# Kernel optimization log

Hardware: AMD Instinct MI355X
Metric: run time of the kernel (lower is better)

The kernel has to match this reference:

```python
import jax, jax.numpy as jnp
import numpy as np

T, B, IN, H, OUT, L = 2048, 128, 64, 128, 32, 2


def setup_inputs() -> dict:
    key = jax.random.key(0)
    ks = jax.random.split(key, 8)
    s_in = 1.0 / np.sqrt(H)  # torch LSTM init scale: U(-1/sqrt(H), 1/sqrt(H))
    inp = {
        "x": jax.random.normal(ks[0], (T, B, IN), dtype=jnp.float32),
        "w_ih0": jax.random.uniform(ks[1], (4 * H, IN), minval=-s_in, maxval=s_in, dtype=jnp.float32),
        "w_hh0": jax.random.uniform(ks[2], (4 * H, H), minval=-s_in, maxval=s_in, dtype=jnp.float32),
        "w_ih1": jax.random.uniform(ks[3], (4 * H, H), minval=-s_in, maxval=s_in, dtype=jnp.float32),
        "w_hh1": jax.random.uniform(ks[4], (4 * H, H), minval=-s_in, maxval=s_in, dtype=jnp.float32),
        "fc_w": jax.random.uniform(ks[5], (OUT, H), minval=-s_in, maxval=s_in, dtype=jnp.float32),
        "fc_b": jax.random.uniform(ks[6], (OUT,), minval=-s_in, maxval=s_in, dtype=jnp.float32),
    }
    return inp


def _lstm_layer(x, w_ih, w_hh):
    # x: [T, B, D]; gate order i, f, g, o (PyTorch convention), no bias.
    x_proj = jnp.einsum("tbd,gd->tbg", x, w_ih)  # [T, B, 4H] precomputed input GEMM
    h0 = jnp.zeros((x.shape[1], H), dtype=x.dtype)
    c0 = jnp.zeros((x.shape[1], H), dtype=x.dtype)

    def step(carry, xp):
        h, c = carry
        gates = xp + h @ w_hh.T  # [B, 4H]
        i, f, g, o = jnp.split(gates, 4, axis=-1)
        i = jax.nn.sigmoid(i)
        f = jax.nn.sigmoid(f)
        g = jnp.tanh(g)
        o = jax.nn.sigmoid(o)
        c = f * c + i * g
        h = o * jnp.tanh(c)
        return (h, c), h

    (h_n, c_n), ys = jax.lax.scan(step, (h0, c0), x_proj)
    return ys, h_n, c_n


def reference(x, w_ih0, w_hh0, w_ih1, w_hh1, fc_w, fc_b):
    y0, h0n, c0n = _lstm_layer(x, w_ih0, w_hh0)
    y1, h1n, c1n = _lstm_layer(y0, w_ih1, w_hh1)
    out = jnp.einsum("tbh,oh->tbo", y1, fc_w) + fc_b  # [T, B, OUT]
    h_n = jnp.stack([h0n, h1n], axis=0)  # [L, B, H]
    c_n = jnp.stack([c0n, c1n], axis=0)
    return out, (h_n, c_n)
```

## Files before the change

### kernel.cpp

```cpp
#include <hip/hip_runtime.h>

#define T_ 2048
#define B_ 128
#define IN_ 64
#define H_ 128
#define OUT_ 32
#define CH_ 32
#define RING_ 2

typedef _Float16 half8 __attribute__((ext_vector_type(8)));
typedef _Float16 half4v __attribute__((ext_vector_type(4)));
typedef float float4v __attribute__((ext_vector_type(4)));

#define XSTR 144
#define HSTR 272
#define GRP_ELEMS ((size_t)RING_ * CH_ * 16 * 128)
#define RING_BYTES ((size_t)8 * GRP_ELEMS * 2)

#define NLOG2E  (-1.4426950408889634f)
#define C2LOG2E ( 2.8853900817779268f)

__device__ __forceinline__ float exp2_hw(float x) {
#if __has_builtin(__builtin_amdgcn_exp2f)
  return __builtin_amdgcn_exp2f(x);
#else
  return exp2f(x);
#endif
}
__device__ __forceinline__ float sigm_pre(float xs) {
  return __builtin_amdgcn_rcpf(1.0f + exp2_hw(xs));
}
__device__ __forceinline__ float tanh_pre(float xs) {
  return fmaf(-2.0f, __builtin_amdgcn_rcpf(1.0f + exp2_hw(xs)), 1.0f);
}
__device__ __forceinline__ float tanh_c(float x) { return tanh_pre(x * C2LOG2E); }

__device__ __forceinline__ float4v sigm4(float4v a) {
  float4v r;
#pragma unroll
  for (int i = 0; i < 4; ++i) r[i] = sigm_pre(a[i]);
  return r;
}
__device__ __forceinline__ float4v tanh4(float4v a) {
  float4v r;
#pragma unroll
  for (int i = 0; i < 4; ++i) r[i] = tanh_pre(a[i]);
  return r;
}

__device__ __forceinline__ void bar_light() {
  __builtin_amdgcn_sched_barrier(0);
  asm volatile("s_waitcnt lgkmcnt(0)" ::: "memory");
  __builtin_amdgcn_s_barrier();
  asm volatile("" ::: "memory");
  __builtin_amdgcn_sched_barrier(0);
}
__device__ __forceinline__ void bar_full() {
  __builtin_amdgcn_sched_barrier(0);
  asm volatile("s_waitcnt vmcnt(0) lgkmcnt(0)" ::: "memory");
  __builtin_amdgcn_s_barrier();
  asm volatile("" ::: "memory");
  __builtin_amdgcn_sched_barrier(0);
}

__device__ __forceinline__ half8 make_afrag(const float* __restrict__ W, int K, int row, int col, float sc) {
  const float* p = W + (size_t)row * K + col;
  float4 a = *(const float4*)p;
  float4 b = *(const float4*)(p + 4);
  half8 h;
  h[0]=(_Float16)(a.x*sc); h[1]=(_Float16)(a.y*sc); h[2]=(_Float16)(a.z*sc); h[3]=(_Float16)(a.w*sc);
  h[4]=(_Float16)(b.x*sc); h[5]=(_Float16)(b.y*sc); h[6]=(_Float16)(b.z*sc); h[7]=(_Float16)(b.w*sc);
  return h;
}

__device__ __forceinline__ void wait_ge(int* p, int want) {
  while (__hip_atomic_load(p, __ATOMIC_RELAXED, __HIP_MEMORY_SCOPE_AGENT) < want)
    __builtin_amdgcn_s_sleep(2);
}

__global__ void ring_init(int* f) { if (threadIdx.x < 16) f[threadIdx.x] = 0; }

__global__ __launch_bounds__(512) void lstm_wavefront(
    const float* __restrict__ x, const float* __restrict__ w_ih0,
    const float* __restrict__ w_hh0, const float* __restrict__ w_ih1,
    const float* __restrict__ w_hh1, const float* __restrict__ fc_w,
    const float* __restrict__ fc_b, float* __restrict__ out, char* __restrict__ ws)
{
  const int tid  = threadIdx.x, lane = tid & 63, w = tid >> 6;
  const int quad = lane >> 4, n = lane & 15;
  const int g = blockIdx.x & 7, layer = blockIdx.x >> 3;
  _Float16* ring = (_Float16*)ws + (size_t)g * GRP_ELEMS;
  int* flag     = (int*)(ws + RING_BYTES) + g;
  int* consumed = (int*)(ws + RING_BYTES) + 8 + g;

  __shared__ char sh_x[4 * 16 * XSTR];
  __shared__ char sh_h[2 * 16 * HSTR];

  const size_t hn_base = (size_t)T_ * B_ * OUT_;
  float4v c = {0.f, 0.f, 0.f, 0.f};
  float hf[4] = {0.f, 0.f, 0.f, 0.f};

  for (int i = tid; i < 2 * 16 * HSTR / 4; i += 512) ((unsigned*)sh_h)[i] = 0u;

  if (layer == 0) {
    half8 a_x[4][2], a_h[4][4];
#pragma unroll
    for (int gt = 0; gt < 4; ++gt) {
      const float sc = (gt == 2) ? C2LOG2E : NLOG2E;
      const int row = gt * H_ + w * 16 + n;
#pragma unroll
      for (int kt = 0; kt < 2; ++kt) a_x[gt][kt] = make_afrag(w_ih0, IN_, row, kt * 32 + quad * 8, sc);
#pragma unroll
      for (int kt = 0; kt < 4; ++kt) a_h[gt][kt] = make_afrag(w_hh0, H_, row, kt * 32 + quad * 8, sc);
    }
    const int xn = tid >> 5, xk = (tid & 31) * 2;
#pragma unroll
    for (int k = 0; k < 2; ++k) {
      float2 xv = *(const float2*)(x + ((size_t)k * B_ + g * 16 + xn) * IN_ + xk);
      _Float16* d = (_Float16*)(sh_x + k * 16 * XSTR + xn * XSTR + xk * 2);
      d[0] = (_Float16)xv.x; d[1] = (_Float16)xv.y;
    }
    __syncthreads();
    half4v hh_def = {0, 0, 0, 0};

    for (int t = 0; t < T_; ++t) {
      const int ck = t >> 5, s = t & (CH_ - 1);
      if (s == 0 && ck >= RING_) wait_ge(consumed, ck - 1);
      if (t > 0)
        *(half4v*)(ring + ((size_t)((t - 1) & 63) * 16 + n) * 128 + w * 16 + quad * 4) = hh_def;
      float2 xv = make_float2(0.f, 0.f);
      if (t + 2 < T_) xv = *(const float2*)(x + ((size_t)(t + 2) * B_ + g * 16 + xn) * IN_ + xk);

      half8 Bx[2], Bh[4];
#pragma unroll
      for (int kt = 0; kt < 2; ++kt)
        Bx[kt] = *(const half8*)(sh_x + (t & 3) * 16 * XSTR + n * XSTR + (kt * 32 + quad * 8) * 2);
#pragma unroll
      for (int kt = 0; kt < 4; ++kt)
        Bh[kt] = *(const half8*)(sh_h + (t & 1) * 16 * HSTR + n * HSTR + (kt * 32 + quad * 8) * 2);

      float4v ga[4];
#pragma unroll
      for (int gt = 0; gt < 4; ++gt) {
        float4v acc = {0.f, 0.f, 0.f, 0.f};
        acc = __builtin_amdgcn_mfma_f32_16x16x32_f16(a_x[gt][0], Bx[0], acc, 0, 0, 0);
        acc = __builtin_amdgcn_mfma_f32_16x16x32_f16(a_x[gt][1], Bx[1], acc, 0, 0, 0);
#pragma unroll
        for (int kt = 0; kt < 4; ++kt)
          acc = __builtin_amdgcn_mfma_f32_16x16x32_f16(a_h[gt][kt], Bh[kt], acc, 0, 0, 0);
        ga[gt] = (gt == 2) ? tanh4(acc) : sigm4(acc);
      }
      half4v hh;
#pragma unroll
      for (int r = 0; r < 4; ++r) {
        c[r] = fmaf(ga[1][r], c[r], ga[0][r] * ga[2][r]);
        hf[r] = ga[3][r] * tanh_c(c[r]);
        hh[r] = (_Float16)hf[r];
      }
      *(half4v*)(sh_h + ((t & 1) ^ 1) * 16 * HSTR + n * HSTR + (w * 16 + quad * 4) * 2) = hh;
      hh_def = hh;
      if (t + 2 < T_) {
        _Float16* d = (_Float16*)(sh_x + ((t + 2) & 3) * 16 * XSTR + xn * XSTR + xk * 2);
        d[0] = (_Float16)xv.x; d[1] = (_Float16)xv.y;
      }
      if (s == 0) bar_full(); else bar_light();
      if (tid == 0 && s == 0 && t > 0) {
        __builtin_amdgcn_fence(__ATOMIC_RELEASE, "agent");
        __hip_atomic_store(flag, ck, __ATOMIC_RELAXED, __HIP_MEMORY_SCOPE_AGENT);
      }
    }
    *(half4v*)(ring + ((size_t)((T_ - 1) & 63) * 16 + n) * 128 + w * 16 + quad * 4) = hh_def;
    bar_full();
    if (tid == 0) {
      __builtin_amdgcn_fence(__ATOMIC_RELEASE, "agent");
      __hip_atomic_store(flag, T_ / CH_, __ATOMIC_RELAXED, __HIP_MEMORY_SCOPE_AGENT);
    }
    {
      float* hn = out + hn_base;
      float* cn = out + hn_base + 2 * (size_t)B_ * H_;
      size_t idx = (size_t)(g * 16 + n) * H_ + w * 16 + quad * 4;
      *(float4*)(hn + idx) = make_float4(hf[0], hf[1], hf[2], hf[3]);
      *(float4*)(cn + idx) = make_float4(c[0], c[1], c[2], c[3]);
    }
  } else {
    half8 a_i[4][4], a_h[4][4], a_fc[4];
#pragma unroll
    for (int gt = 0; gt < 4; ++gt) {
      const float sc = (gt == 2) ? C2LOG2E : NLOG2E;
      const int row = gt * H_ + w * 16 + n;
#pragma unroll
      for (int kt = 0; kt < 4; ++kt) {
        a_i[gt][kt] = make_afrag(w_ih1, H_, row, kt * 32 + quad * 8, sc);
        a_h[gt][kt] = make_afrag(w_hh1, H_, row, kt * 32 + quad * 8, sc);
      }
    }
    float4 fb = make_float4(0.f, 0.f, 0.f, 0.f);
    if (w < 2) {
#pragma unroll
      for (int kt = 0; kt < 4; ++kt) a_fc[kt] = make_afrag(fc_w, H_, w * 16 + n, kt * 32 + quad * 8, 1.0f);
      fb = *(const float4*)(fc_b + w * 16 + quad * 4);
    }
    __syncthreads();
    half8 By[4];

    for (int t = 0; t < T_; ++t) {
      const int ck = t >> 5, s = t & (CH_ - 1);
      if (s == 0) {
        wait_ge(flag, ck + 1);
        __builtin_amdgcn_fence(__ATOMIC_ACQUIRE, "agent");
        const _Float16* yp = ring + ((size_t)(t & 63) * 16 + n) * 128 + quad * 8;
#pragma unroll
        for (int kt = 0; kt < 4; ++kt) By[kt] = *(const half8*)(yp + kt * 32);
      }
      half8 Bh[4];
#pragma unroll
      for (int kt = 0; kt < 4; ++kt)
        Bh[kt] = *(const half8*)(sh_h + (t & 1) * 16 * HSTR + n * HSTR + (kt * 32 + quad * 8) * 2);
      if (w < 2 && t > 0) {
        float4v af = {0.f, 0.f, 0.f, 0.f};
#pragma unroll
        for (int kt = 0; kt < 4; ++kt)
          af = __builtin_amdgcn_mfma_f32_16x16x32_f16(a_fc[kt], Bh[kt], af, 0, 0, 0);
        float* op = out + ((size_t)(t - 1) * B_ + g * 16 + n) * OUT_ + w * 16 + quad * 4;
        *(float4*)op = make_float4(af[0] + fb.x, af[1] + fb.y, af[2] + fb.z, af[3] + fb.w);
      }
      float4v ga[4];
#pragma unroll
      for (int gt = 0; gt < 4; ++gt) {
        float4v acc = {0.f, 0.f, 0.f, 0.f};
#pragma unroll
        for (int kt = 0; kt < 4; ++kt)
          acc = __builtin_amdgcn_mfma_f32_16x16x32_f16(a_i[gt][kt], By[kt], acc, 0, 0, 0);
#pragma unroll
        for (int kt = 0; kt < 4; ++kt)
          acc = __builtin_amdgcn_mfma_f32_16x16x32_f16(a_h[gt][kt], Bh[kt], acc, 0, 0, 0);
        ga[gt] = (gt == 2) ? tanh4(acc) : sigm4(acc);
      }
      half8 Byn[4];
      const bool pf = (s != CH_ - 1) && (t + 1 < T_);
      if (pf) {
        const _Float16* yp = ring + ((size_t)((t + 1) & 63) * 16 + n) * 128 + quad * 8;
#pragma unroll
        for (int kt = 0; kt < 4; ++kt) Byn[kt] = *(const half8*)(yp + kt * 32);
      }
      half4v hh;
#pragma unroll
      for (int r = 0; r < 4; ++r) {
        c[r] = fmaf(ga[1][r], c[r], ga[0][r] * ga[2][r]);
        hf[r] = ga[3][r] * tanh_c(c[r]);
        hh[r] = (_Float16)hf[r];
      }
      *(half4v*)(sh_h + ((t & 1) ^ 1) * 16 * HSTR + n * HSTR + (w * 16 + quad * 4) * 2) = hh;
      bar_light();
      if (s == CH_ - 1 && tid == 0) {
        __builtin_amdgcn_fence(__ATOMIC_RELEASE, "agent");
        __hip_atomic_store(consumed, ck + 1, __ATOMIC_RELAXED, __HIP_MEMORY_SCOPE_AGENT);
      }
      if (pf) {
#pragma unroll
        for (int kt = 0; kt < 4; ++kt) By[kt] = Byn[kt];
      }
    }
    if (w < 2) {
      float4v af = {0.f, 0.f, 0.f, 0.f};
#pragma unroll
      for (int kt = 0; kt < 4; ++kt) {
        half8 Bh = *(const half8*)(sh_h + (T_ & 1) * 16 * HSTR + n * HSTR + (kt * 32 + quad * 8) * 2);
        af = __builtin_amdgcn_mfma_f32_16x16x32_f16(a_fc[kt], Bh, af, 0, 0, 0);
      }
      float* op = out + ((size_t)(T_ - 1) * B_ + g * 16 + n) * OUT_ + w * 16 + quad * 4;
      *(float4*)op = make_float4(af[0] + fb.x, af[1] + fb.y, af[2] + fb.z, af[3] + fb.w);
    }
    {
      float* hn = out + hn_base + (size_t)B_ * H_;
      float* cn = out + hn_base + 3 * (size_t)B_ * H_;
      size_t idx = (size_t)(g * 16 + n) * H_ + w * 16 + quad * 4;
      *(float4*)(hn + idx) = make_float4(hf[0], hf[1], hf[2], hf[3]);
      *(float4*)(cn + idx) = make_float4(c[0], c[1], c[2], c[3]);
    }
  }
}

extern "C" void kernel_launch(void* const* d_in, const int* in_sizes, int n_in,
                              void* d_out, int out_size, void* d_ws, size_t ws_size,
                              hipStream_t stream) {
  const float* x     = (const float*)d_in[0];
  const float* w_ih0 = (const float*)d_in[1];
  const float* w_hh0 = (const float*)d_in[2];
  const float* w_ih1 = (const float*)d_in[3];
  const float* w_hh1 = (const float*)d_in[4];
  const float* fc_w  = (const float*)d_in[5];
  const float* fc_b  = (const float*)d_in[6];
  char* ws = (char*)d_ws;
  ring_init<<<1, 64, 0, stream>>>((int*)(ws + RING_BYTES));
  lstm_wavefront<<<16, 512, 0, stream>>>(x, w_ih0, w_hh0, w_ih1, w_hh1,
                                         fc_w, fc_b, (float*)d_out, ws);
}
```

Before: 2.938 ms.

## Add two helper waves to offload ring stores, x staging and FC projection

The block grows from 8 to 10 waves. The two extra waves take over side work that used to sit on the recurrent critical path. In layer 0 they copy h from shared memory into the global ring and stage the next x tile. In layer 1 they compute the FC output projection, so the eight gate waves only do the recurrence. This raises per-step barrier participation and may lower register budget per thread under the larger launch bound. Unroll-by-2 hints are also added to the time loops.

```diff
diff --git a/kernel.cpp b/kernel.cpp
--- a/kernel.cpp
+++ b/kernel.cpp
@@ -80,7 +80,7 @@
 
 __global__ void ring_init(int* f) { if (threadIdx.x < 16) f[threadIdx.x] = 0; }
 
-__global__ __launch_bounds__(512) void lstm_wavefront(
+__global__ __launch_bounds__(640) void lstm_wavefront(
     const float* __restrict__ x, const float* __restrict__ w_ih0,
     const float* __restrict__ w_hh0, const float* __restrict__ w_ih1,
     const float* __restrict__ w_hh1, const float* __restrict__ fc_w,
@@ -100,68 +100,85 @@
   float4v c = {0.f, 0.f, 0.f, 0.f};
   float hf[4] = {0.f, 0.f, 0.f, 0.f};
 
-  for (int i = tid; i < 2 * 16 * HSTR / 4; i += 512) ((unsigned*)sh_h)[i] = 0u;
+  for (int i = tid; i < 2 * 16 * HSTR / 4; i += 640) ((unsigned*)sh_h)[i] = 0u;
 
   if (layer == 0) {
     half8 a_x[4][2], a_h[4][4];
-#pragma unroll
-    for (int gt = 0; gt < 4; ++gt) {
-      const float sc = (gt == 2) ? C2LOG2E : NLOG2E;
-      const int row = gt * H_ + w * 16 + n;
-#pragma unroll
-      for (int kt = 0; kt < 2; ++kt) a_x[gt][kt] = make_afrag(w_ih0, IN_, row, kt * 32 + quad * 8, sc);
-#pragma unroll
-      for (int kt = 0; kt < 4; ++kt) a_h[gt][kt] = make_afrag(w_hh0, H_, row, kt * 32 + quad * 8, sc);
-    }
-    const int xn = tid >> 5, xk = (tid & 31) * 2;
-#pragma unroll
-    for (int k = 0; k < 2; ++k) {
-      float2 xv = *(const float2*)(x + ((size_t)k * B_ + g * 16 + xn) * IN_ + xk);
-      _Float16* d = (_Float16*)(sh_x + k * 16 * XSTR + xn * XSTR + xk * 2);
-      d[0] = (_Float16)xv.x; d[1] = (_Float16)xv.y;
+    if (w < 8) {
+#pragma unroll
+      for (int gt = 0; gt < 4; ++gt) {
+        const float sc = (gt == 2) ? C2LOG2E : NLOG2E;
+        const int row = gt * H_ + w * 16 + n;
+#pragma unroll
+        for (int kt = 0; kt < 2; ++kt) a_x[gt][kt] = make_afrag(w_ih0, IN_, row, kt * 32 + quad * 8, sc);
+#pragma unroll
+        for (int kt = 0; kt < 4; ++kt) a_h[gt][kt] = make_afrag(w_hh0, H_, row, kt * 32 + quad * 8, sc);
+      }
+    } else {
+      const int r = (tid - 512) >> 3, cx = ((tid - 512) & 7) * 8;
+#pragma unroll
+      for (int k = 0; k < 2; ++k) {
+        const float* xp = x + ((size_t)k * B_ + g * 16 + r) * IN_ + cx;
+        float4 a = *(const float4*)xp, b = *(const float4*)(xp + 4);
+        half8 hx;
+        hx[0]=(_Float16)a.x; hx[1]=(_Float16)a.y; hx[2]=(_Float16)a.z; hx[3]=(_Float16)a.w;
+        hx[4]=(_Float16)b.x; hx[5]=(_Float16)b.y; hx[6]=(_Float16)b.z; hx[7]=(_Float16)b.w;
+        *(half8*)(sh_x + k * 16 * XSTR + r * XSTR + cx * 2) = hx;
+      }
     }
     __syncthreads();
-    half4v hh_def = {0, 0, 0, 0};
-
+
+#pragma unroll 2
     for (int t = 0; t < T_; ++t) {
       const int ck = t >> 5, s = t & (CH_ - 1);
       if (s == 0 && ck >= RING_) wait_ge(consumed, ck - 1);
-      if (t > 0)
-        *(half4v*)(ring + ((size_t)((t - 1) & 63) * 16 + n) * 128 + w * 16 + quad * 4) = hh_def;
-      float2 xv = make_float2(0.f, 0.f);
-      if (t + 2 < T_) xv = *(const float2*)(x + ((size_t)(t + 2) * B_ + g * 16 + xn) * IN_ + xk);
-
-      half8 Bx[2], Bh[4];
-#pragma unroll
-      for (int kt = 0; kt < 2; ++kt)
-        Bx[kt] = *(const half8*)(sh_x + (t & 3) * 16 * XSTR + n * XSTR + (kt * 32 + quad * 8) * 2);
-#pragma unroll
-      for (int kt = 0; kt < 4; ++kt)
-        Bh[kt] = *(const half8*)(sh_h + (t & 1) * 16 * HSTR + n * HSTR + (kt * 32 + quad * 8) * 2);
-
-      float4v ga[4];
-#pragma unroll
-      for (int gt = 0; gt < 4; ++gt) {
-        float4v acc = {0.f, 0.f, 0.f, 0.f};
-        acc = __builtin_amdgcn_mfma_f32_16x16x32_f16(a_x[gt][0], Bx[0], acc, 0, 0, 0);
-        acc = __builtin_amdgcn_mfma_f32_16x16x32_f16(a_x[gt][1], Bx[1], acc, 0, 0, 0);
+      if (w < 8) {
+        half8 Bx[2], Bh[4];
+#pragma unroll
+        for (int kt = 0; kt < 2; ++kt)
+          Bx[kt] = *(const half8*)(sh_x + (t & 3) * 16 * XSTR + n * XSTR + (kt * 32 + quad * 8) * 2);
 #pragma unroll
         for (int kt = 0; kt < 4; ++kt)
-          acc = __builtin_amdgcn_mfma_f32_16x16x32_f16(a_h[gt][kt], Bh[kt], acc, 0, 0, 0);
-        ga[gt] = (gt == 2) ? tanh4(acc) : sigm4(acc);
-      }
-      half4v hh;
-#pragma unroll
-      for (int r = 0; r < 4; ++r) {
-        c[r] = fmaf(ga[1][r], c[r], ga[0][r] * ga[2][r]);
-        hf[r] = ga[3][r] * tanh_c(c[r]);
-        hh[r] = (_Float16)hf[r];
-      }
-      *(half4v*)(sh_h + ((t & 1) ^ 1) * 16 * HSTR + n * HSTR + (w * 16 + quad * 4) * 2) = hh;
-      hh_def = hh;
-      if (t + 2 < T_) {
-        _Float16* d = (_Float16*)(sh_x + ((t + 2) & 3) * 16 * XSTR + xn * XSTR + xk * 2);
-        d[0] = (_Float16)xv.x; d[1] = (_Float16)xv.y;
+          Bh[kt] = *(const half8*)(sh_h + (t & 1) * 16 * HSTR + n * HSTR + (kt * 32 + quad * 8) * 2);
+        float4v ga[4];
+#pragma unroll
+        for (int gt = 0; gt < 4; ++gt) {
+          float4v acc = {0.f, 0.f, 0.f, 0.f};
+          acc = __builtin_amdgcn_mfma_f32_16x16x32_f16(a_x[gt][0], Bx[0], acc, 0, 0, 0);
+          acc = __builtin_amdgcn_mfma_f32_16x16x32_f16(a_x[gt][1], Bx[1], acc, 0, 0, 0);
+#pragma unroll
+          for (int kt = 0; kt < 4; ++kt)
+            acc = __builtin_amdgcn_mfma_f32_16x16x32_f16(a_h[gt][kt], Bh[kt], acc, 0, 0, 0);
+          ga[gt] = (gt == 2) ? tanh4(acc) : sigm4(acc);
+        }
+        half4v hh;
+#pragma unroll
+        for (int r = 0; r < 4; ++r) {
+          c[r] = fmaf(ga[1][r], c[r], ga[0][r] * ga[2][r]);
+          hf[r] = ga[3][r] * tanh_c(c[r]);
+          hh[r] = (_Float16)hf[r];
+        }
+        *(half4v*)(sh_h + ((t & 1) ^ 1) * 16 * HSTR + n * HSTR + (w * 16 + quad * 4) * 2) = hh;
+      } else {
+        const int r = (tid - 512) >> 3;
+        if (t > 0) {
+          const int c16 = ((tid - 512) & 7) * 16;
+          const char* sp = sh_h + (t & 1) * 16 * HSTR + r * HSTR + c16 * 2;
+          half8 v0 = *(const half8*)sp;
+          half8 v1 = *(const half8*)(sp + 16);
+          _Float16* rp = ring + ((size_t)((t - 1) & 63) * 16 + r) * 128 + c16;
+          *(half8*)rp = v0;
+          *(half8*)(rp + 8) = v1;
+        }
+        if (t + 2 < T_) {
+          const int cx = ((tid - 512) & 7) * 8;
+          const float* xp = x + ((size_t)(t + 2) * B_ + g * 16 + r) * IN_ + cx;
+          float4 a = *(const float4*)xp, b = *(const float4*)(xp + 4);
+          half8 hx;
+          hx[0]=(_Float16)a.x; hx[1]=(_Float16)a.y; hx[2]=(_Float16)a.z; hx[3]=(_Float16)a.w;
+          hx[4]=(_Float16)b.x; hx[5]=(_Float16)b.y; hx[6]=(_Float16)b.z; hx[7]=(_Float16)b.w;
+          *(half8*)(sh_x + ((t + 2) & 3) * 16 * XSTR + r * XSTR + cx * 2) = hx;
+        }
       }
       if (s == 0) bar_full(); else bar_light();
       if (tid == 0 && s == 0 && t > 0) {
@@ -169,13 +186,21 @@
         __hip_atomic_store(flag, ck, __ATOMIC_RELAXED, __HIP_MEMORY_SCOPE_AGENT);
       }
     }
-    *(half4v*)(ring + ((size_t)((T_ - 1) & 63) * 16 + n) * 128 + w * 16 + quad * 4) = hh_def;
+    if (w >= 8) {
+      const int r = (tid - 512) >> 3, c16 = ((tid - 512) & 7) * 16;
+      const char* sp = sh_h + r * HSTR + c16 * 2;
+      half8 v0 = *(const half8*)sp;
+      half8 v1 = *(const half8*)(sp + 16);
+      _Float16* rp = ring + ((size_t)((T_ - 1) & 63) * 16 + r) * 128 + c16;
+      *(half8*)rp = v0;
+      *(half8*)(rp + 8) = v1;
+    }
     bar_full();
     if (tid == 0) {
       __builtin_amdgcn_fence(__ATOMIC_RELEASE, "agent");
       __hip_atomic_store(flag, T_ / CH_, __ATOMIC_RELAXED, __HIP_MEMORY_SCOPE_AGENT);
     }
-    {
+    if (w < 8) {
       float* hn = out + hn_base;
       float* cn = out + hn_base + 2 * (size_t)B_ * H_;
       size_t idx = (size_t)(g * 16 + n) * H_ + w * 16 + quad * 4;
@@ -184,94 +209,106 @@
     }
   } else {
     half8 a_i[4][4], a_h[4][4], a_fc[4];
-#pragma unroll
-    for (int gt = 0; gt < 4; ++gt) {
-      const float sc = (gt == 2) ? C2LOG2E : NLOG2E;
-      const int row = gt * H_ + w * 16 + n;
-#pragma unroll
-      for (int kt = 0; kt < 4; ++kt) {
-        a_i[gt][kt] = make_afrag(w_ih1, H_, row, kt * 32 + quad * 8, sc);
-        a_h[gt][kt] = make_afrag(w_hh1, H_, row, kt * 32 + quad * 8, sc);
-      }
-    }
     float4 fb = make_float4(0.f, 0.f, 0.f, 0.f);
-    if (w < 2) {
-#pragma unroll
-      for (int kt = 0; kt < 4; ++kt) a_fc[kt] = make_afrag(fc_w, H_, w * 16 + n, kt * 32 + quad * 8, 1.0f);
-      fb = *(const float4*)(fc_b + w * 16 + quad * 4);
+    if (w < 8) {
+#pragma unroll
+      for (int gt = 0; gt < 4; ++gt) {
+        const float sc = (gt == 2) ? C2LOG2E : NLOG2E;
+        const int row = gt * H_ + w * 16 + n;
+#pragma unroll
+        for (int kt = 0; kt < 4; ++kt) {
+          a_i[gt][kt] = make_afrag(w_ih1, H_, row, kt * 32 + quad * 8, sc);
+          a_h[gt][kt] = make_afrag(w_hh1, H_, row, kt * 32 + quad * 8, sc);
+        }
+      }
+    } else {
+#pragma unroll
+      for (int kt = 0; kt < 4; ++kt)
+        a_fc[kt] = make_afrag(fc_w, H_, (w & 1) * 16 + n, kt * 32 + quad * 8, 1.0f);
+      fb = *(const float4*)(fc_b + (w & 1) * 16 + quad * 4);
     }
     __syncthreads();
     half8 By[4];
 
+#pragma unroll 2
     for (int t = 0; t < T_; ++t) {
       const int ck = t >> 5, s = t & (CH_ - 1);
       if (s == 0) {
         wait_ge(flag, ck + 1);
         __builtin_amdgcn_fence(__ATOMIC_ACQUIRE, "agent");
-        const _Float16* yp = ring + ((size_t)(t & 63) * 16 + n) * 128 + quad * 8;
-#pragma unroll
-        for (int kt = 0; kt < 4; ++kt) By[kt] = *(const half8*)(yp + kt * 32);
-      }
-      half8 Bh[4];
-#pragma unroll
-      for (int kt = 0; kt < 4; ++kt)
-        Bh[kt] = *(const half8*)(sh_h + (t & 1) * 16 * HSTR + n * HSTR + (kt * 32 + quad * 8) * 2);
-      if (w < 2 && t > 0) {
-        float4v af = {0.f, 0.f, 0.f, 0.f};
+        if (w < 8) {
+          const _Float16* yp = ring + ((size_t)(t & 63) * 16 + n) * 128 + quad * 8;
+#pragma unroll
+          for (int kt = 0; kt < 4; ++kt) By[kt] = *(const half8*)(yp + kt * 32);
+        }
+      }
+      if (w < 8) {
+        half8 Bh[4];
 #pragma unroll
         for (int kt = 0; kt < 4; ++kt)
-          af = __builtin_amdgcn_mfma_f32_16x16x32_f16(a_fc[kt], Bh[kt], af, 0, 0, 0);
-        float* op = out + ((size_t)(t - 1) * B_ + g * 16 + n) * OUT_ + w * 16 + quad * 4;
-        *(float4*)op = make_float4(af[0] + fb.x, af[1] + fb.y, af[2] + fb.z, af[3] + fb.w);
-      }
-      float4v ga[4];
-#pragma unroll
-      for (int gt = 0; gt < 4; ++gt) {
-        float4v acc = {0.f, 0.f, 0.f, 0.f};
-#pragma unroll
-        for (int kt = 0; kt < 4; ++kt)
-          acc = __builtin_amdgcn_mfma_f32_16x16x32_f16(a_i[gt][kt], By[kt], acc, 0, 0, 0);
-#pragma unroll
-        for (int kt = 0; kt < 4; ++kt)
-          acc = __builtin_amdgcn_mfma_f32_16x16x32_f16(a_h[gt][kt], Bh[kt], acc, 0, 0, 0);
-        ga[gt] = (gt == 2) ? tanh4(acc) : sigm4(acc);
-      }
-      half8 Byn[4];
-      const bool pf = (s != CH_ - 1) && (t + 1 < T_);
-      if (pf) {
-        const _Float16* yp = ring + ((size_t)((t + 1) & 63) * 16 + n) * 128 + quad * 8;
-#pragma unroll
-        for (int kt = 0; kt < 4; ++kt) Byn[kt] = *(const half8*)(yp + kt * 32);
-      }
-      half4v hh;
-#pragma unroll
-      for (int r = 0; r < 4; ++r) {
-        c[r] = fmaf(ga[1][r], c[r], ga[0][r] * ga[2][r]);
-        hf[r] = ga[3][r] * tanh_c(c[r]);
-        hh[r] = (_Float16)hf[r];
-      }
-      *(half4v*)(sh_h + ((t & 1) ^ 1) * 16 * HSTR + n * HSTR + (w * 16 + quad * 4) * 2) = hh;
+          Bh[kt] = *(const half8*)(sh_h + (t & 1) * 16 * HSTR + n * HSTR + (kt * 32 + quad * 8) * 2);
+        half8 Byn[4];
+        const bool pf = (s != CH_ - 1) && (t + 1 < T_);
+        if (pf) {
+          const _Float16* yp = ring + ((size_t)((t + 1) & 63) * 16 + n) * 128 + quad * 8;
+#pragma unroll
+          for (int kt = 0; kt < 4; ++kt) Byn[kt] = *(const half8*)(yp + kt * 32);
+        }
+        float4v ga[4];
+#pragma unroll
+        for (int gt = 0; gt < 4; ++gt) {
+          float4v acc = {0.f, 0.f, 0.f, 0.f};
+#pragma unroll
+          for (int kt = 0; kt < 4; ++kt)
+            acc = __builtin_amdgcn_mfma_f32_16x16x32_f16(a_i[gt][kt], By[kt], acc, 0, 0, 0);
+#pragma unroll
+          for (int kt = 0; kt < 4; ++kt)
+            acc = __builtin_amdgcn_mfma_f32_16x16x32_f16(a_h[gt][kt], Bh[kt], acc, 0, 0, 0);
+          ga[gt] = (gt == 2) ? tanh4(acc) : sigm4(acc);
+        }
+        half4v hh;
+#pragma unroll
+        for (int r = 0; r < 4; ++r) {
+          c[r] = fmaf(ga[1][r], c[r], ga[0][r] * ga[2][r]);
+          hf[r] = ga[3][r] * tanh_c(c[r]);
+          hh[r] = (_Float16)hf[r];
+        }
+        *(half4v*)(sh_h + ((t & 1) ^ 1) * 16 * HSTR + n * HSTR + (w * 16 + quad * 4) * 2) = hh;
+        if (pf) {
+#pragma unroll
+          for (int kt = 0; kt < 4; ++kt) By[kt] = Byn[kt];
+        }
+      } else {
+        if (t > 0) {
+          half8 Bf[4];
+#pragma unroll
+          for (int kt = 0; kt < 4; ++kt)
+            Bf[kt] = *(const half8*)(sh_h + (t & 1) * 16 * HSTR + n * HSTR + (kt * 32 + quad * 8) * 2);
+          float4v af = {0.f, 0.f, 0.f, 0.f};
+#pragma unroll
+          for (int kt = 0; kt < 4; ++kt)
+            af = __builtin_amdgcn_mfma_f32_16x16x32_f16(a_fc[kt], Bf[kt], af, 0, 0, 0);
+          float* op = out + ((size_t)(t - 1) * B_ + g * 16 + n) * OUT_ + (w & 1) * 16 + quad * 4;
+          *(float4*)op = make_float4(af[0] + fb.x, af[1] + fb.y, af[2] + fb.z, af[3] + fb.w);
+        }
+      }
       bar_light();
       if (s == CH_ - 1 && tid == 0) {
         __builtin_amdgcn_fence(__ATOMIC_RELEASE, "agent");
         __hip_atomic_store(consumed, ck + 1, __ATOMIC_RELAXED, __HIP_MEMORY_SCOPE_AGENT);
       }
-      if (pf) {
-#pragma unroll
-        for (int kt = 0; kt < 4; ++kt) By[kt] = Byn[kt];
-      }
-    }
-    if (w < 2) {
+    }
+    if (w >= 8) {
       float4v af = {0.f, 0.f, 0.f, 0.f};
 #pragma unroll
       for (int kt = 0; kt < 4; ++kt) {
-        half8 Bh = *(const half8*)(sh_h + (T_ & 1) * 16 * HSTR + n * HSTR + (kt * 32 + quad * 8) * 2);
-        af = __builtin_amdgcn_mfma_f32_16x16x32_f16(a_fc[kt], Bh, af, 0, 0, 0);
-      }
-      float* op = out + ((size_t)(T_ - 1) * B_ + g * 16 + n) * OUT_ + w * 16 + quad * 4;
+        half8 Bf = *(const half8*)(sh_h + n * HSTR + (kt * 32 + quad * 8) * 2);
+        af = __builtin_amdgcn_mfma_f32_16x16x32_f16(a_fc[kt], Bf, af, 0, 0, 0);
+      }
+      float* op = out + ((size_t)(T_ - 1) * B_ + g * 16 + n) * OUT_ + (w & 1) * 16 + quad * 4;
       *(float4*)op = make_float4(af[0] + fb.x, af[1] + fb.y, af[2] + fb.z, af[3] + fb.w);
     }
-    {
+    if (w < 8) {
       float* hn = out + hn_base + (size_t)B_ * H_;
       float* cn = out + hn_base + 3 * (size_t)B_ * H_;
       size_t idx = (size_t)(g * 16 + n) * H_ + w * 16 + quad * 4;
@@ -293,6 +330,6 @@
   const float* fc_b  = (const float*)d_in[6];
   char* ws = (char*)d_ws;
   ring_init<<<1, 64, 0, stream>>>((int*)(ws + RING_BYTES));
-  lstm_wavefront<<<16, 512, 0, stream>>>(x, w_ih0, w_hh0, w_ih1, w_hh1,
+  lstm_wavefront<<<16, 640, 0, stream>>>(x, w_ih0, w_hh0, w_ih1, w_hh1,
                                          fc_w, fc_b, (float*)d_out, ws);
 }
```

After: 8.154 ms. +177.5%, slower.
